# Kernel optimization log

Measured on AMD Instinct MI355X. Metric: run time of the kernel, lower is better.

The kernel has to match this reference:

```python
import jax, jax.numpy as jnp
import numpy as np
import math

ALPHA = 1.0
EPS = 1e-8
PI = math.pi


def setup_inputs() -> dict:
    key = jax.random.key(0)
    k1, k2 = jax.random.split(key)
    B, L, P = 32, 8, 1024
    pred_keypoints = jax.random.normal(k1, (B, L, P, 2), dtype=jnp.float32)
    gt_keypoints = jax.random.normal(k2, (B, L, P, 2), dtype=jnp.float32)
    return {"pred_keypoints": pred_keypoints, "gt_keypoints": gt_keypoints}


def _segments(pts):
    """pts: [..., P, 2] -> (dl [..., S, 2], mid [..., S, 2]) with S = P-1.
    Faithful to torch: tangent = diff/sqrt(|diff|^2+eps), dl = tangent*|diff| (norm w/o eps)."""
    diff = pts[..., 1:, :] - pts[..., :-1, :]
    sumsq = jnp.sum(diff * diff, axis=-1)
    seg_len = jnp.sqrt(sumsq)                       # torch.norm(p2-p1)
    scale = seg_len / jnp.sqrt(sumsq + EPS)          # |dl| factor vs raw diff
    dl = diff * scale[..., None]
    mid = 0.5 * (pts[..., 1:, :] + pts[..., :-1, :])
    return dl, mid


def _self_energy(dl, mid):
    """dl, mid: [B, L, S, 2] -> per-lane self energy [B, L]."""
    S = dl.shape[-2]
    line = jnp.sum(jnp.linalg.norm(dl, axis=-1), axis=-1) / (8.0 * PI)
    dots = jnp.einsum('blid,bljd->blij', dl, dl)                 # [B,L,S,S]
    r = jnp.linalg.norm(mid[..., None, :, :] - mid[..., :, None, :], axis=-1) + EPS
    mask = jnp.triu(jnp.ones((S, S), dtype=bool), k=1)           # i < j pairs only
    pair = jnp.sum(jnp.where(mask, dots / (8.0 * PI * r), 0.0), axis=(-1, -2))
    return line + pair


def _interaction_energy(dl_p, mid_p, dl_g, mid_g):
    """-> per-lane interaction energy [B, L] (note dot(dl1, -dl2) in torch)."""
    dots = jnp.einsum('blid,bljd->blij', dl_p, dl_g)             # [B,L,Sp,Sg]
    r = jnp.linalg.norm(mid_g[..., None, :, :] - mid_p[..., :, None, :], axis=-1) + EPS
    return jnp.sum(-dots / (4.0 * PI * r), axis=(-1, -2))


def reference(pred_keypoints, gt_keypoints):
    B = pred_keypoints.shape[0]
    dl_p, mid_p = _segments(pred_keypoints)
    dl_g, mid_g = _segments(gt_keypoints)
    e_self_p = _self_energy(dl_p, mid_p)
    e_self_g = _self_energy(dl_g, mid_g)
    e_int = _interaction_energy(dl_p, mid_p, dl_g, mid_g)
    lane_loss = e_self_p + e_self_g - 2.0 * ALPHA * e_int        # [B, L]
    return jnp.sum(lane_loss) / B
```

## Files before the change

kernel.cpp:

```cpp
#include <hip/hip_runtime.h>
#include <math.h>

constexpr int B = 32;
constexpr int L = 8;
constexpr int P = 1024;
constexpr int S = 1023;
constexpr float EPS = 1e-8f;

#define INV8PI 0.039788735772973836
#define INV2PI 0.15915494309189535

__device__ __forceinline__ float4 make_seg(const float2* __restrict__ pts, int i) {
    float2 a = pts[i];
    float2 b = pts[i + 1];
    float dx = b.x - a.x, dy = b.y - a.y;
    float s2 = dx * dx + dy * dy;
    float len = sqrtf(s2);
    float scale = len / sqrtf(s2 + EPS);
    float4 r;
    r.x = dx * scale;
    r.y = dy * scale;
    r.z = 0.5f * (a.x + b.x);
    r.w = 0.5f * (a.y + b.y);
    return r;
}

__device__ __forceinline__ float pair_term(float rx, float ry, float mz, float mw,
                                           const float4& c) {
    float rdx = c.z - mz;
    float rdy = c.w - mw;
    float d2  = fmaf(rdx, rdx, fmaf(rdy, rdy, 1e-30f));
    float dot = fmaf(rx, c.x, ry * c.y);
    return dot * __builtin_amdgcn_rsqf(d2);
}

__global__ __launch_bounds__(256, 8) void
pair_kernel(const float* __restrict__ pred, const float* __restrict__ gt,
            double* __restrict__ acc) {
    __shared__ float4 cs[1024];
    __shared__ double wsum[4];

    const int lane  = blockIdx.y;
    const int part  = blockIdx.x;
    const int mtype = part >> 2;
    const int rtile = part & 3;
    const int tid   = threadIdx.x;

    const float2* rowpts = (const float2*)(mtype == 1 ? gt : pred) + (size_t)lane * P;
    const float2* colpts = (const float2*)(mtype == 0 ? pred : gt) + (size_t)lane * P;

    for (int j = tid; j < S; j += 256) {
        cs[j] = make_seg(colpts, j);
    }

    const int i = rtile * 256 + tid;
    float4 rs;
    if (i < S) {
        rs = make_seg(rowpts, i);
    } else {
        rs.x = 0.f; rs.y = 0.f; rs.z = 0.f; rs.w = 0.f;
    }
    __syncthreads();

    const float rx = rs.x, ry = rs.y, mz = rs.z, mw = rs.w;

    double accd = 0.0;

    if (mtype < 2 && rtile == 0) {
        float lf = 0.0f;
        for (int j = tid; j < S; j += 256) {
            float4 s = cs[j];
            lf += sqrtf(s.x * s.x + s.y * s.y);
        }
        accd += (double)lf;
    }

    int jmain;
    if (mtype == 2) {
        jmain = 0;
    } else {
        const int ws = i & ~63;
        const int je = (ws + 64 < S) ? (ws + 64) : S;
        float pf = 0.0f;
        for (int j = ws; j < je; ++j) {
            float t = pair_term(rx, ry, mz, mw, cs[j]);
            pf += (j > i) ? t : 0.0f;
        }
        accd += (double)pf;
        jmain = ws + 64;
    }

    for (int j0 = jmain; j0 < S; j0 += 256) {
        const int je = (j0 + 256 < S) ? (j0 + 256) : S;
        float accf = 0.0f;
#pragma unroll 4
        for (int j = j0; j < je; ++j) {
            accf += pair_term(rx, ry, mz, mw, cs[j]);
        }
        accd += (double)accf;
    }

    for (int off = 32; off; off >>= 1) accd += __shfl_down(accd, off, 64);
    if ((tid & 63) == 0) wsum[tid >> 6] = accd;
    __syncthreads();
    if (tid == 0) {
        double tot = wsum[0] + wsum[1] + wsum[2] + wsum[3];
        double coef = (mtype == 2) ? INV2PI : INV8PI;
        atomicAdd(acc, tot * coef);
    }
}

__global__ void finalize_kernel(const double* __restrict__ acc, float* __restrict__ out) {
    out[0] = (float)(acc[0] / (double)B);
}

extern "C" void kernel_launch(void* const* d_in, const int* in_sizes, int n_in,
                              void* d_out, int out_size, void* d_ws, size_t ws_size,
                              hipStream_t stream) {
    const float* pred = (const float*)d_in[0];
    const float* gt   = (const float*)d_in[1];
    double* acc = (double*)d_ws;

    hipMemsetAsync(d_ws, 0, sizeof(double), stream);

    dim3 grid(12, 256);
    pair_kernel<<<grid, dim3(256), 0, stream>>>(pred, gt, acc);
    finalize_kernel<<<1, 1, 0, stream>>>(acc, (float*)d_out);
}
```

Baseline: 224.0 us.

## Split segment LDS to SoA and use packed float2 math in inner loop

Measured after the change: 230.9 us. +3.1%, slower.

```diff
diff --git a/kernel.cpp b/kernel.cpp
--- a/kernel.cpp
+++ b/kernel.cpp
@@ -9,6 +9,8 @@
 
 #define INV8PI 0.039788735772973836
 #define INV2PI 0.15915494309189535
+
+typedef float f32x2 __attribute__((ext_vector_type(2)));
 
 __device__ __forceinline__ float4 make_seg(const float2* __restrict__ pts, int i) {
     float2 a = pts[i];
@@ -25,19 +27,13 @@
     return r;
 }
 
-__device__ __forceinline__ float pair_term(float rx, float ry, float mz, float mw,
-                                           const float4& c) {
-    float rdx = c.z - mz;
-    float rdy = c.w - mw;
-    float d2  = fmaf(rdx, rdx, fmaf(rdy, rdy, 1e-30f));
-    float dot = fmaf(rx, c.x, ry * c.y);
-    return dot * __builtin_amdgcn_rsqf(d2);
-}
-
 __global__ __launch_bounds__(256, 8) void
 pair_kernel(const float* __restrict__ pred, const float* __restrict__ gt,
             double* __restrict__ acc) {
-    __shared__ float4 cs[1024];
+    __shared__ float sdlx[1024];
+    __shared__ float sdly[1024];
+    __shared__ float smx[1024];
+    __shared__ float smy[1024];
     __shared__ double wsum[4];
 
     const int lane  = blockIdx.y;
@@ -50,27 +46,37 @@
     const float2* colpts = (const float2*)(mtype == 0 ? pred : gt) + (size_t)lane * P;
 
     for (int j = tid; j < S; j += 256) {
-        cs[j] = make_seg(colpts, j);
+        float4 s = make_seg(colpts, j);
+        sdlx[j] = s.x; sdly[j] = s.y; smx[j] = s.z; smy[j] = s.w;
+    }
+    if (tid == 0) {
+        sdlx[1023] = 0.f; sdly[1023] = 0.f; smx[1023] = 0.f; smy[1023] = 0.f;
     }
 
     const int i = rtile * 256 + tid;
-    float4 rs;
+    float rx, ry, mz, mw;
     if (i < S) {
-        rs = make_seg(rowpts, i);
+        float4 rs = make_seg(rowpts, i);
+        rx = rs.x; ry = rs.y; mz = rs.z; mw = rs.w;
     } else {
-        rs.x = 0.f; rs.y = 0.f; rs.z = 0.f; rs.w = 0.f;
+        rx = 0.f; ry = 0.f; mz = 0.f; mw = 0.f;
     }
     __syncthreads();
 
-    const float rx = rs.x, ry = rs.y, mz = rs.z, mw = rs.w;
+    const f32x2 rx2 = {rx, rx}, ry2 = {ry, ry}, mz2 = {mz, mz}, mw2 = {mw, mw};
+    const f32x2 eps2 = {1e-30f, 1e-30f};
+
+    const f32x2* pdlx = (const f32x2*)sdlx;
+    const f32x2* pdly = (const f32x2*)sdly;
+    const f32x2* pmx  = (const f32x2*)smx;
+    const f32x2* pmy  = (const f32x2*)smy;
 
     double accd = 0.0;
 
     if (mtype < 2 && rtile == 0) {
         float lf = 0.0f;
         for (int j = tid; j < S; j += 256) {
-            float4 s = cs[j];
-            lf += sqrtf(s.x * s.x + s.y * s.y);
+            lf += sqrtf(sdlx[j] * sdlx[j] + sdly[j] * sdly[j]);
         }
         accd += (double)lf;
     }
@@ -83,21 +89,36 @@
         const int je = (ws + 64 < S) ? (ws + 64) : S;
         float pf = 0.0f;
         for (int j = ws; j < je; ++j) {
-            float t = pair_term(rx, ry, mz, mw, cs[j]);
+            float rdx = smx[j] - mz;
+            float rdy = smy[j] - mw;
+            float d2  = fmaf(rdx, rdx, fmaf(rdy, rdy, 1e-30f));
+            float dot = fmaf(rx, sdlx[j], ry * sdly[j]);
+            float t   = dot * __builtin_amdgcn_rsqf(d2);
             pf += (j > i) ? t : 0.0f;
         }
         accd += (double)pf;
         jmain = ws + 64;
     }
 
-    for (int j0 = jmain; j0 < S; j0 += 256) {
-        const int je = (j0 + 256 < S) ? (j0 + 256) : S;
-        float accf = 0.0f;
+    for (int j0 = jmain; j0 < 1024; j0 += 256) {
+        const int je = (j0 + 256 < 1024) ? (j0 + 256) : 1024;
+        f32x2 accf = {0.f, 0.f};
 #pragma unroll 4
-        for (int j = j0; j < je; ++j) {
-            accf += pair_term(rx, ry, mz, mw, cs[j]);
+        for (int jp = j0 >> 1; jp < (je >> 1); ++jp) {
+            f32x2 cx = pdlx[jp];
+            f32x2 cy = pdly[jp];
+            f32x2 cmx = pmx[jp];
+            f32x2 cmy = pmy[jp];
+            f32x2 rdx = cmx - mz2;
+            f32x2 rdy = cmy - mw2;
+            f32x2 d2  = rdx * rdx + (rdy * rdy + eps2);
+            f32x2 dot = rx2 * cx + ry2 * cy;
+            f32x2 rs2;
+            rs2.x = __builtin_amdgcn_rsqf(d2.x);
+            rs2.y = __builtin_amdgcn_rsqf(d2.y);
+            accf += dot * rs2;
         }
-        accd += (double)accf;
+        accd += (double)accf.x + (double)accf.y;
     }
 
     for (int off = 32; off; off >>= 1) accd += __shfl_down(accd, off, 64);
```
